# Kernel optimization log

Hardware: AMD Instinct MI355X
Metric: run time of the kernel (lower is better)

The kernel has to match this reference:

```python
import jax, jax.numpy as jnp
import numpy as np

B, S, E = 8, 4096, 256
NQ, F = 8, 1024


def setup_inputs() -> dict:
    key = jax.random.key(0)
    k1, k2, k3, k4 = jax.random.split(key, 4)
    x = jax.random.normal(k1, (B, S, E), dtype=jnp.float32)
    theta = jax.random.normal(k2, (NQ,), dtype=jnp.float32)
    W1 = jax.random.normal(k3, (F, NQ), dtype=jnp.float32) * (1.0 / np.sqrt(NQ))
    W2 = jax.random.normal(k4, (E, F), dtype=jnp.float32) * (1.0 / np.sqrt(F))
    return {"x": x, "theta": theta, "W1": W1, "W2": W2}


def reference(x, theta, W1, W2):
    # Quantum layer: per wire w, |0> -> RX(x_w) -> RY(theta_w) -> <Z>.
    # No entangling gates => product state; exact closed form:
    #   <Z_w> = cos(x_w) * cos(theta_w)
    nq = theta.shape[0]
    q = jnp.cos(x[..., :nq]) * jnp.cos(theta)           # [B, S, nq]
    # dropout is identity in eval mode (p interpreted at inference)
    h = jax.nn.relu(jnp.einsum('bsq,fq->bsf', q, W1))   # [B, S, F]
    return jnp.einsum('bsf,ef->bse', h, W2)             # [B, S, E]
```

## Files before the change

kernel.cpp:

```cpp
#include <hip/hip_runtime.h>
#include <hip/hip_bf16.h>

typedef __attribute__((ext_vector_type(8)))  short  short8_t;
typedef __attribute__((ext_vector_type(4)))  float  float4_t;
typedef __attribute__((ext_vector_type(16))) float  f32x16_t;
typedef __attribute__((ext_vector_type(4)))  int    int4_t;
typedef __attribute__((ext_vector_type(2)))  unsigned int uint2_t;

__device__ __forceinline__ unsigned short f2bf(float f) {
    unsigned int u = __builtin_bit_cast(unsigned int, f);
    u += 0x7FFFu + ((u >> 16) & 1u);
    return (unsigned short)(u >> 16);
}
__device__ __forceinline__ unsigned int cvtpk(float a, float b) {
    return (unsigned int)f2bf(a) | ((unsigned int)f2bf(b) << 16);
}
__device__ __forceinline__ unsigned int cvtpk_hw(float a, float b) {
    unsigned int r;
    asm("v_cvt_pk_bf16_f32 %0, %1, %2" : "=v"(r) : "v"(a), "v"(b));
    return r;
}
__device__ __forceinline__ void plane32_swap(unsigned int& a, unsigned int& b) {
    asm("v_permlane32_swap_b32 %0, %1" : "+v"(a), "+v"(b));
}

__global__ void prep_kernel(const float* __restrict__ W2, const float* __restrict__ W1,
                            unsigned short* __restrict__ W2t, unsigned short* __restrict__ W1b) {
    const int bid = blockIdx.x, tid = threadIdx.x;
    if (bid < 128) {
        const int g   = bid * 256 + tid;
        const int l   = g & 63;
        const int pos = g >> 6;
        const int ks  = pos >> 3;
        const int et  = pos & 7;
        const int e   = et * 32 + (l & 31);
        const int f0  = ks * 16 + (l >> 5) * 8;
        const float* src = W2 + (size_t)e * 1024 + f0;
        const float4_t v0 = *reinterpret_cast<const float4_t*>(src);
        const float4_t v1 = *reinterpret_cast<const float4_t*>(src + 4);
        int4_t p;
        p[0] = (int)cvtpk(v0[0], v0[1]);
        p[1] = (int)cvtpk(v0[2], v0[3]);
        p[2] = (int)cvtpk(v1[0], v1[1]);
        p[3] = (int)cvtpk(v1[2], v1[3]);
        *reinterpret_cast<int4_t*>(W2t + (size_t)g * 8) = p;
    } else {
        const int base = tid * 32;
        #pragma unroll
        for (int it = 0; it < 8; ++it) {
            const float4_t v = *reinterpret_cast<const float4_t*>(W1 + base + it * 4);
            uint2_t p;
            p[0] = cvtpk(v[0], v[1]);
            p[1] = cvtpk(v[2], v[3]);
            *reinterpret_cast<uint2_t*>(W1b + base + it * 4) = p;
        }
    }
}

template <bool WSOK>
__global__ __launch_bounds__(256, 4)
void ffq_kernel(const float* __restrict__ x,
                const float* __restrict__ theta,
                const float* __restrict__ W1f,
                const unsigned short* __restrict__ W1b,
                const float* __restrict__ W2f,
                const unsigned short* __restrict__ W2t,
                float* __restrict__ out)
{
    __shared__ __align__(16) unsigned short hL[32 * 32 * 8];

    const int tid  = threadIdx.x;
    const int lane = tid & 63;
    const int w    = tid >> 6;
    const int bid  = blockIdx.x;
    const int rowbase = bid * 32;
    const int m  = lane & 31;
    const int hi = lane >> 5;

    short8_t qf = {0,0,0,0,0,0,0,0};
    if (lane < 32) {
        const float* xp = x + (size_t)(rowbase + m) * 256;
        const float4_t x0 = *reinterpret_cast<const float4_t*>(xp);
        const float4_t x1 = *reinterpret_cast<const float4_t*>(xp + 4);
        float qv[8];
        #pragma unroll
        for (int j = 0; j < 4; ++j) {
            qv[j]     = __cosf(x0[j]) * __cosf(theta[j]);
            qv[4 + j] = __cosf(x1[j]) * __cosf(theta[4 + j]);
        }
        int4_t pq;
        pq[0] = (int)cvtpk(qv[0], qv[1]);
        pq[1] = (int)cvtpk(qv[2], qv[3]);
        pq[2] = (int)cvtpk(qv[4], qv[5]);
        pq[3] = (int)cvtpk(qv[6], qv[7]);
        qf = __builtin_bit_cast(short8_t, pq);
    }

    f32x16_t acc0 = {0}, acc1 = {0};
    #pragma unroll
    for (int i = 0; i < 16; ++i) { acc0[i] = 0.f; acc1[i] = 0.f; }
    f32x16_t zz = acc0;

    if constexpr (WSOK) {
        #pragma unroll 1
        for (int c = 0; c < 4; ++c) {
            __syncthreads();

            #pragma unroll
            for (int i = 0; i < 2; ++i) {
                const int ftl = w * 2 + i;
                const int ftg = c * 8 + ftl;
                const short8_t af = *reinterpret_cast<const short8_t*>(
                    (const char*)W1b + (size_t)(ftg * 32 + m) * 16 + hi * 16);
                const f32x16_t d = __builtin_amdgcn_mfma_f32_32x32x16_bf16(af, qf, zz, 0, 0, 0);
                #pragma unroll
                for (int b = 0; b < 4; ++b) {
                    uint2_t pk;
                    pk[0] = cvtpk_hw(fmaxf(d[4*b+0], 0.f), fmaxf(d[4*b+1], 0.f));
                    pk[1] = cvtpk_hw(fmaxf(d[4*b+2], 0.f), fmaxf(d[4*b+3], 0.f));
                    *reinterpret_cast<uint2_t*>(
                        &hL[((ftl * 4 + b) * 32 + m) * 8 + hi * 4]) = pk;
                }
            }

            __syncthreads();

            #pragma unroll 4
            for (int ksl = 0; ksl < 16; ++ksl) {
                const short8_t bf = *reinterpret_cast<const short8_t*>(
                    &hL[((ksl * 2 + hi) * 32 + m) * 8]);
                const int ks = c * 16 + ksl;
                const short8_t a0 = *reinterpret_cast<const short8_t*>(
                    W2t + (size_t)(ks * 8 + 2 * w)     * 512 + lane * 8);
                const short8_t a1 = *reinterpret_cast<const short8_t*>(
                    W2t + (size_t)(ks * 8 + 2 * w + 1) * 512 + lane * 8);
                acc0 = __builtin_amdgcn_mfma_f32_32x32x16_bf16(a0, bf, acc0, 0, 0, 0);
                acc1 = __builtin_amdgcn_mfma_f32_32x32x16_bf16(a1, bf, acc1, 0, 0, 0);
            }
        }
    } else {
        short8_t bf0, bf1;
        auto htr = [&](short8_t af) {
            const f32x16_t d = __builtin_amdgcn_mfma_f32_32x32x16_bf16(af, qf, zz, 0, 0, 0);
            unsigned int U00 = cvtpk_hw(fmaxf(d[0],  0.f), fmaxf(d[1],  0.f));
            unsigned int U01 = cvtpk_hw(fmaxf(d[2],  0.f), fmaxf(d[3],  0.f));
            unsigned int U10 = cvtpk_hw(fmaxf(d[4],  0.f), fmaxf(d[5],  0.f));
            unsigned int U11 = cvtpk_hw(fmaxf(d[6],  0.f), fmaxf(d[7],  0.f));
            unsigned int U20 = cvtpk_hw(fmaxf(d[8],  0.f), fmaxf(d[9],  0.f));
            unsigned int U21 = cvtpk_hw(fmaxf(d[10], 0.f), fmaxf(d[11], 0.f));
            unsigned int U30 = cvtpk_hw(fmaxf(d[12], 0.f), fmaxf(d[13], 0.f));
            unsigned int U31 = cvtpk_hw(fmaxf(d[14], 0.f), fmaxf(d[15], 0.f));
            plane32_swap(U00, U10);
            plane32_swap(U01, U11);
            plane32_swap(U20, U30);
            plane32_swap(U21, U31);
            int4_t p0; p0[0]=(int)U00; p0[1]=(int)U01; p0[2]=(int)U10; p0[3]=(int)U11;
            int4_t p1; p1[0]=(int)U20; p1[1]=(int)U21; p1[2]=(int)U30; p1[3]=(int)U31;
            bf0 = __builtin_bit_cast(short8_t, p0);
            bf1 = __builtin_bit_cast(short8_t, p1);
        };
        for (int s = 0; s < 32; ++s) {
            const float* ws = W1f + (size_t)(s * 32 + m) * 8;
            const float4_t a0 = *reinterpret_cast<const float4_t*>(ws);
            const float4_t a1 = *reinterpret_cast<const float4_t*>(ws + 4);
            int4_t pa;
            pa[0] = (int)cvtpk(a0[0], a0[1]);
            pa[1] = (int)cvtpk(a0[2], a0[3]);
            pa[2] = (int)cvtpk(a1[0], a1[1]);
            pa[3] = (int)cvtpk(a1[2], a1[3]);
            htr(__builtin_bit_cast(short8_t, pa));
            int4_t fr[4];
            #pragma unroll
            for (int kw = 0; kw < 2; ++kw)
                #pragma unroll
                for (int et = 0; et < 2; ++et) {
                    const int e = w * 64 + et * 32 + m;
                    const float* p = W2f + (size_t)e * 1024 + (s * 32 + kw * 16) + hi * 8;
                    const float4_t v0 = *reinterpret_cast<const float4_t*>(p);
                    const float4_t v1 = *reinterpret_cast<const float4_t*>(p + 4);
                    int4_t pb;
                    pb[0] = (int)cvtpk(v0[0], v0[1]);
                    pb[1] = (int)cvtpk(v0[2], v0[3]);
                    pb[2] = (int)cvtpk(v1[0], v1[1]);
                    pb[3] = (int)cvtpk(v1[2], v1[3]);
                    fr[kw * 2 + et] = pb;
                }
            const short8_t f0 = __builtin_bit_cast(short8_t, fr[0]);
            const short8_t f1 = __builtin_bit_cast(short8_t, fr[1]);
            const short8_t f2 = __builtin_bit_cast(short8_t, fr[2]);
            const short8_t f3 = __builtin_bit_cast(short8_t, fr[3]);
            acc0 = __builtin_amdgcn_mfma_f32_32x32x16_bf16(f0, bf0, acc0, 0, 0, 0);
            acc1 = __builtin_amdgcn_mfma_f32_32x32x16_bf16(f1, bf0, acc1, 0, 0, 0);
            acc0 = __builtin_amdgcn_mfma_f32_32x32x16_bf16(f2, bf1, acc0, 0, 0, 0);
            acc1 = __builtin_amdgcn_mfma_f32_32x32x16_bf16(f3, bf1, acc1, 0, 0, 0);
        }
    }

    {
        float* orow = out + (size_t)(rowbase + m) * 256 + w * 64 + hi * 4;
        #define STORE_ET(ACC, ET) do {                                            \
            _Pragma("unroll")                                                     \
            for (int rq = 0; rq < 4; ++rq) {                                      \
                float4_t v;                                                       \
                v[0] = ACC[4*rq+0]; v[1] = ACC[4*rq+1];                           \
                v[2] = ACC[4*rq+2]; v[3] = ACC[4*rq+3];                           \
                *reinterpret_cast<float4_t*>(orow + (ET) * 32 + rq * 8) = v;      \
            } } while (0)
        STORE_ET(acc0, 0);
        STORE_ET(acc1, 1);
        #undef STORE_ET
    }
}

extern "C" void kernel_launch(void* const* d_in, const int* in_sizes, int n_in,
                              void* d_out, int out_size, void* d_ws, size_t ws_size,
                              hipStream_t stream) {
    const float* x     = (const float*)d_in[0];
    const float* theta = (const float*)d_in[1];
    const float* W1    = (const float*)d_in[2];
    const float* W2    = (const float*)d_in[3];
    float* out = (float*)d_out;

    const size_t need = (size_t)(256 * 1024 + 1024 * 8) * sizeof(unsigned short) + 16;
    const bool wsok = (ws_size >= need);

    if (wsok) {
        unsigned short* W2t = (unsigned short*)d_ws;
        unsigned short* W1b = W2t + 256 * 1024;
        prep_kernel<<<129, 256, 0, stream>>>(W2, W1, W2t, W1b);
        ffq_kernel<true><<<1024, 256, 0, stream>>>(x, theta, nullptr, W1b, nullptr, W2t, out);
    } else {
        ffq_kernel<false><<<1024, 256, 0, stream>>>(x, theta, W1, nullptr, W2, nullptr, out);
    }
}
```

Before: 39.52 us.

## Split output columns across two blocks per row tile to double grid parallelism

Each block now computes only half of the output embedding columns for its 32-row tile, doubling the grid to 2048 blocks and raising the launch-bounds occupancy hint to 8. Each wave holds one accumulator instead of two, reducing register pressure. The aim is better latency hiding and more waves in flight per CU. The cost is that the first-layer hidden activations (MFMA, ReLU, LDS staging) and the input cosine computation are recomputed in both blocks.

Result: slower. 42.48 us (+7.5%).

```diff
diff --git a/kernel.cpp b/kernel.cpp
--- a/kernel.cpp
+++ b/kernel.cpp
@@ -58,7 +58,7 @@
 }
 
 template <bool WSOK>
-__global__ __launch_bounds__(256, 4)
+__global__ __launch_bounds__(256, 8)
 void ffq_kernel(const float* __restrict__ x,
                 const float* __restrict__ theta,
                 const float* __restrict__ W1f,
@@ -73,7 +73,8 @@
     const int lane = tid & 63;
     const int w    = tid >> 6;
     const int bid  = blockIdx.x;
-    const int rowbase = bid * 32;
+    const int ct      = bid & 1;
+    const int rowbase = (bid >> 1) * 32;
     const int m  = lane & 31;
     const int hi = lane >> 5;
 
@@ -96,9 +97,9 @@
         qf = __builtin_bit_cast(short8_t, pq);
     }
 
-    f32x16_t acc0 = {0}, acc1 = {0};
+    f32x16_t acc0 = {0};
     #pragma unroll
-    for (int i = 0; i < 16; ++i) { acc0[i] = 0.f; acc1[i] = 0.f; }
+    for (int i = 0; i < 16; ++i) acc0[i] = 0.f;
     f32x16_t zz = acc0;
 
     if constexpr (WSOK) {
@@ -131,11 +132,8 @@
                     &hL[((ksl * 2 + hi) * 32 + m) * 8]);
                 const int ks = c * 16 + ksl;
                 const short8_t a0 = *reinterpret_cast<const short8_t*>(
-                    W2t + (size_t)(ks * 8 + 2 * w)     * 512 + lane * 8);
-                const short8_t a1 = *reinterpret_cast<const short8_t*>(
-                    W2t + (size_t)(ks * 8 + 2 * w + 1) * 512 + lane * 8);
+                    W2t + (size_t)(ks * 8 + ct * 4 + w) * 512 + lane * 8);
                 acc0 = __builtin_amdgcn_mfma_f32_32x32x16_bf16(a0, bf, acc0, 0, 0, 0);
-                acc1 = __builtin_amdgcn_mfma_f32_32x32x16_bf16(a1, bf, acc1, 0, 0, 0);
             }
         }
     } else {
@@ -169,46 +167,33 @@
             pa[2] = (int)cvtpk(a1[0], a1[1]);
             pa[3] = (int)cvtpk(a1[2], a1[3]);
             htr(__builtin_bit_cast(short8_t, pa));
-            int4_t fr[4];
+            const int e = ct * 128 + w * 32 + m;
             #pragma unroll
-            for (int kw = 0; kw < 2; ++kw)
-                #pragma unroll
-                for (int et = 0; et < 2; ++et) {
-                    const int e = w * 64 + et * 32 + m;
-                    const float* p = W2f + (size_t)e * 1024 + (s * 32 + kw * 16) + hi * 8;
-                    const float4_t v0 = *reinterpret_cast<const float4_t*>(p);
-                    const float4_t v1 = *reinterpret_cast<const float4_t*>(p + 4);
-                    int4_t pb;
-                    pb[0] = (int)cvtpk(v0[0], v0[1]);
-                    pb[1] = (int)cvtpk(v0[2], v0[3]);
-                    pb[2] = (int)cvtpk(v1[0], v1[1]);
-                    pb[3] = (int)cvtpk(v1[2], v1[3]);
-                    fr[kw * 2 + et] = pb;
-                }
-            const short8_t f0 = __builtin_bit_cast(short8_t, fr[0]);
-            const short8_t f1 = __builtin_bit_cast(short8_t, fr[1]);
-            const short8_t f2 = __builtin_bit_cast(short8_t, fr[2]);
-            const short8_t f3 = __builtin_bit_cast(short8_t, fr[3]);
-            acc0 = __builtin_amdgcn_mfma_f32_32x32x16_bf16(f0, bf0, acc0, 0, 0, 0);
-            acc1 = __builtin_amdgcn_mfma_f32_32x32x16_bf16(f1, bf0, acc1, 0, 0, 0);
-            acc0 = __builtin_amdgcn_mfma_f32_32x32x16_bf16(f2, bf1, acc0, 0, 0, 0);
-            acc1 = __builtin_amdgcn_mfma_f32_32x32x16_bf16(f3, bf1, acc1, 0, 0, 0);
+            for (int kw = 0; kw < 2; ++kw) {
+                const float* p = W2f + (size_t)e * 1024 + (s * 32 + kw * 16) + hi * 8;
+                const float4_t v0 = *reinterpret_cast<const float4_t*>(p);
+                const float4_t v1 = *reinterpret_cast<const float4_t*>(p + 4);
+                int4_t pb;
+                pb[0] = (int)cvtpk(v0[0], v0[1]);
+                pb[1] = (int)cvtpk(v0[2], v0[3]);
+                pb[2] = (int)cvtpk(v1[0], v1[1]);
+                pb[3] = (int)cvtpk(v1[2], v1[3]);
+                const short8_t fb = __builtin_bit_cast(short8_t, pb);
+                acc0 = __builtin_amdgcn_mfma_f32_32x32x16_bf16(
+                    fb, (kw == 0) ? bf0 : bf1, acc0, 0, 0, 0);
+            }
         }
     }
 
     {
-        float* orow = out + (size_t)(rowbase + m) * 256 + w * 64 + hi * 4;
-        #define STORE_ET(ACC, ET) do {                                            \
-            _Pragma("unroll")                                                     \
-            for (int rq = 0; rq < 4; ++rq) {                                      \
-                float4_t v;                                                       \
-                v[0] = ACC[4*rq+0]; v[1] = ACC[4*rq+1];                           \
-                v[2] = ACC[4*rq+2]; v[3] = ACC[4*rq+3];                           \
-                *reinterpret_cast<float4_t*>(orow + (ET) * 32 + rq * 8) = v;      \
-            } } while (0)
-        STORE_ET(acc0, 0);
-        STORE_ET(acc1, 1);
-        #undef STORE_ET
+        float* orow = out + (size_t)(rowbase + m) * 256 + ct * 128 + w * 32 + hi * 4;
+        #pragma unroll
+        for (int rq = 0; rq < 4; ++rq) {
+            float4_t v;
+            v[0] = acc0[4*rq+0]; v[1] = acc0[4*rq+1];
+            v[2] = acc0[4*rq+2]; v[3] = acc0[4*rq+3];
+            *reinterpret_cast<float4_t*>(orow + rq * 8) = v;
+        }
     }
 }
 
@@ -228,8 +213,8 @@
         unsigned short* W2t = (unsigned short*)d_ws;
         unsigned short* W1b = W2t + 256 * 1024;
         prep_kernel<<<129, 256, 0, stream>>>(W2, W1, W2t, W1b);
-        ffq_kernel<true><<<1024, 256, 0, stream>>>(x, theta, nullptr, W1b, nullptr, W2t, out);
+        ffq_kernel<true><<<2048, 256, 0, stream>>>(x, theta, nullptr, W1b, nullptr, W2t, out);
     } else {
-        ffq_kernel<false><<<1024, 256, 0, stream>>>(x, theta, W1, nullptr, W2, nullptr, out);
-    }
-}
+        ffq_kernel<false><<<2048, 256, 0, stream>>>(x, theta, W1, nullptr, W2, nullptr, out);
+    }
+}
```

## Retile FFN kernel to 128-row blocks with waves covering half of E

Applied to the files above, without the earlier changes.

Blocks now process 128 rows with 8 waves. Each pair of waves shares a 32-row group's hidden tile, and each wave accumulates 4 output tiles over 128 output columns. This raises reuse of each loaded W2 fragment and of each hidden fragment read from LDS, and halves the hidden-tile work per wave per chunk. In exchange it uses more accumulator registers, makes larger blocks synchronize at barriers, and leaves only 256 blocks, which may underfill the GPU.

Result: slower. 57.30 us (+45.0%).

```diff
diff --git a/kernel.cpp b/kernel.cpp
--- a/kernel.cpp
+++ b/kernel.cpp
@@ -58,7 +58,7 @@
 }
 
 template <bool WSOK>
-__global__ __launch_bounds__(256, 4)
+__global__ __launch_bounds__(512, 2)
 void ffq_kernel(const float* __restrict__ x,
                 const float* __restrict__ theta,
                 const float* __restrict__ W1f,
@@ -67,13 +67,15 @@
                 const unsigned short* __restrict__ W2t,
                 float* __restrict__ out)
 {
-    __shared__ __align__(16) unsigned short hL[32 * 32 * 8];
+    __shared__ __align__(16) unsigned short hL[4][16 * 32 * 8];
 
     const int tid  = threadIdx.x;
     const int lane = tid & 63;
     const int w    = tid >> 6;
+    const int rg   = w >> 1;
+    const int ch   = w & 1;
     const int bid  = blockIdx.x;
-    const int rowbase = bid * 32;
+    const int rowbase = bid * 128 + rg * 32;
     const int m  = lane & 31;
     const int hi = lane >> 5;
 
@@ -96,20 +98,20 @@
         qf = __builtin_bit_cast(short8_t, pq);
     }
 
-    f32x16_t acc0 = {0}, acc1 = {0};
+    f32x16_t acc0 = {0}, acc1 = {0}, acc2 = {0}, acc3 = {0};
     #pragma unroll
-    for (int i = 0; i < 16; ++i) { acc0[i] = 0.f; acc1[i] = 0.f; }
+    for (int i = 0; i < 16; ++i) { acc0[i]=0.f; acc1[i]=0.f; acc2[i]=0.f; acc3[i]=0.f; }
     f32x16_t zz = acc0;
 
     if constexpr (WSOK) {
         #pragma unroll 1
-        for (int c = 0; c < 4; ++c) {
+        for (int c = 0; c < 8; ++c) {
             __syncthreads();
 
             #pragma unroll
             for (int i = 0; i < 2; ++i) {
-                const int ftl = w * 2 + i;
-                const int ftg = c * 8 + ftl;
+                const int ftl = ch * 2 + i;
+                const int ftg = c * 4 + ftl;
                 const short8_t af = *reinterpret_cast<const short8_t*>(
                     (const char*)W1b + (size_t)(ftg * 32 + m) * 16 + hi * 16);
                 const f32x16_t d = __builtin_amdgcn_mfma_f32_32x32x16_bf16(af, qf, zz, 0, 0, 0);
@@ -119,23 +121,27 @@
                     pk[0] = cvtpk_hw(fmaxf(d[4*b+0], 0.f), fmaxf(d[4*b+1], 0.f));
                     pk[1] = cvtpk_hw(fmaxf(d[4*b+2], 0.f), fmaxf(d[4*b+3], 0.f));
                     *reinterpret_cast<uint2_t*>(
-                        &hL[((ftl * 4 + b) * 32 + m) * 8 + hi * 4]) = pk;
+                        &hL[rg][((ftl * 4 + b) * 32 + m) * 8 + hi * 4]) = pk;
                 }
             }
 
             __syncthreads();
 
-            #pragma unroll 4
-            for (int ksl = 0; ksl < 16; ++ksl) {
+            #pragma unroll 2
+            for (int ksl = 0; ksl < 8; ++ksl) {
                 const short8_t bf = *reinterpret_cast<const short8_t*>(
-                    &hL[((ksl * 2 + hi) * 32 + m) * 8]);
-                const int ks = c * 16 + ksl;
-                const short8_t a0 = *reinterpret_cast<const short8_t*>(
-                    W2t + (size_t)(ks * 8 + 2 * w)     * 512 + lane * 8);
-                const short8_t a1 = *reinterpret_cast<const short8_t*>(
-                    W2t + (size_t)(ks * 8 + 2 * w + 1) * 512 + lane * 8);
+                    &hL[rg][((ksl * 2 + hi) * 32 + m) * 8]);
+                const int ks = c * 8 + ksl;
+                const char* base = (const char*)W2t
+                    + (size_t)ks * 8192 + (size_t)ch * 4096 + (size_t)lane * 16;
+                const short8_t a0 = *reinterpret_cast<const short8_t*>(base);
+                const short8_t a1 = *reinterpret_cast<const short8_t*>(base + 1024);
+                const short8_t a2 = *reinterpret_cast<const short8_t*>(base + 2048);
+                const short8_t a3 = *reinterpret_cast<const short8_t*>(base + 3072);
                 acc0 = __builtin_amdgcn_mfma_f32_32x32x16_bf16(a0, bf, acc0, 0, 0, 0);
                 acc1 = __builtin_amdgcn_mfma_f32_32x32x16_bf16(a1, bf, acc1, 0, 0, 0);
+                acc2 = __builtin_amdgcn_mfma_f32_32x32x16_bf16(a2, bf, acc2, 0, 0, 0);
+                acc3 = __builtin_amdgcn_mfma_f32_32x32x16_bf16(a3, bf, acc3, 0, 0, 0);
             }
         }
     } else {
@@ -169,12 +175,11 @@
             pa[2] = (int)cvtpk(a1[0], a1[1]);
             pa[3] = (int)cvtpk(a1[2], a1[3]);
             htr(__builtin_bit_cast(short8_t, pa));
-            int4_t fr[4];
             #pragma unroll
-            for (int kw = 0; kw < 2; ++kw)
+            for (int i = 0; i < 4; ++i) {
+                const int e = ch * 128 + i * 32 + m;
                 #pragma unroll
-                for (int et = 0; et < 2; ++et) {
-                    const int e = w * 64 + et * 32 + m;
+                for (int kw = 0; kw < 2; ++kw) {
                     const float* p = W2f + (size_t)e * 1024 + (s * 32 + kw * 16) + hi * 8;
                     const float4_t v0 = *reinterpret_cast<const float4_t*>(p);
                     const float4_t v1 = *reinterpret_cast<const float4_t*>(p + 4);
@@ -183,21 +188,19 @@
                     pb[1] = (int)cvtpk(v0[2], v0[3]);
                     pb[2] = (int)cvtpk(v1[0], v1[1]);
                     pb[3] = (int)cvtpk(v1[2], v1[3]);
-                    fr[kw * 2 + et] = pb;
+                    const short8_t fb = __builtin_bit_cast(short8_t, pb);
+                    const short8_t bfx = (kw == 0) ? bf0 : bf1;
+                    if (i == 0) acc0 = __builtin_amdgcn_mfma_f32_32x32x16_bf16(fb, bfx, acc0, 0, 0, 0);
+                    if (i == 1) acc1 = __builtin_amdgcn_mfma_f32_32x32x16_bf16(fb, bfx, acc1, 0, 0, 0);
+                    if (i == 2) acc2 = __builtin_amdgcn_mfma_f32_32x32x16_bf16(fb, bfx, acc2, 0, 0, 0);
+                    if (i == 3) acc3 = __builtin_amdgcn_mfma_f32_32x32x16_bf16(fb, bfx, acc3, 0, 0, 0);
                 }
-            const short8_t f0 = __builtin_bit_cast(short8_t, fr[0]);
-            const short8_t f1 = __builtin_bit_cast(short8_t, fr[1]);
-            const short8_t f2 = __builtin_bit_cast(short8_t, fr[2]);
-            const short8_t f3 = __builtin_bit_cast(short8_t, fr[3]);
-            acc0 = __builtin_amdgcn_mfma_f32_32x32x16_bf16(f0, bf0, acc0, 0, 0, 0);
-            acc1 = __builtin_amdgcn_mfma_f32_32x32x16_bf16(f1, bf0, acc1, 0, 0, 0);
-            acc0 = __builtin_amdgcn_mfma_f32_32x32x16_bf16(f2, bf1, acc0, 0, 0, 0);
-            acc1 = __builtin_amdgcn_mfma_f32_32x32x16_bf16(f3, bf1, acc1, 0, 0, 0);
+            }
         }
     }
 
     {
-        float* orow = out + (size_t)(rowbase + m) * 256 + w * 64 + hi * 4;
+        float* orow = out + (size_t)(rowbase + m) * 256 + ch * 128 + hi * 4;
         #define STORE_ET(ACC, ET) do {                                            \
             _Pragma("unroll")                                                     \
             for (int rq = 0; rq < 4; ++rq) {                                      \
@@ -208,6 +211,8 @@
             } } while (0)
         STORE_ET(acc0, 0);
         STORE_ET(acc1, 1);
+        STORE_ET(acc2, 2);
+        STORE_ET(acc3, 3);
         #undef STORE_ET
     }
 }
@@ -228,8 +233,8 @@
         unsigned short* W2t = (unsigned short*)d_ws;
         unsigned short* W1b = W2t + 256 * 1024;
         prep_kernel<<<129, 256, 0, stream>>>(W2, W1, W2t, W1b);
-        ffq_kernel<true><<<1024, 256, 0, stream>>>(x, theta, nullptr, W1b, nullptr, W2t, out);
+        ffq_kernel<true><<<256, 512, 0, stream>>>(x, theta, nullptr, W1b, nullptr, W2t, out);
     } else {
-        ffq_kernel<false><<<1024, 256, 0, stream>>>(x, theta, W1, nullptr, W2, nullptr, out);
-    }
-}
+        ffq_kernel<false><<<256, 512, 0, stream>>>(x, theta, W1, nullptr, W2, nullptr, out);
+    }
+}
```
